# Performance work log

Measured on AMD Instinct MI355X. Metric: run time of the kernel, lower is better.

## Reference

```python
import jax, jax.numpy as jnp
import numpy as np

B, A, N = 4, 256, 64
NCB, NF, NSB, DIMS = 128, 128, 50, 3
CUTOFF = 5.0
LOG2 = 0.6931471805599453


def ssp(x):
    # shifted softplus: softplus(x) - ln(2)
    return jax.nn.softplus(x) - LOG2


def mlp2(x, W1, b1, W2, b2):
    # Dense(act=ssp) -> Dense(linear)
    return ssp(x @ W1 + b1) @ W2 + b2


def setup_inputs():
    key = jax.random.key(0)
    ks = jax.random.split(key, 32)

    def w(k, shape):
        return jax.random.normal(k, shape, jnp.float32) / np.sqrt(shape[0]).astype(np.float32)

    return {
        "xi": jax.random.normal(ks[0], (B, A, NCB), jnp.float32),
        "r_ij": jax.random.uniform(ks[1], (B, A, N), jnp.float32) * CUTOFF,
        "cos_ij": jax.random.normal(ks[2], (B, A, N, DIMS), jnp.float32),
        "f_ij": jax.random.normal(ks[3], (B, A, N, NSB), jnp.float32),
        "neighbor_mask": jnp.ones((B, A, N), jnp.float32),
        "filt_W1": w(ks[4], (NSB, NF)), "filt_b1": jnp.zeros((NF,), jnp.float32),
        "filt_W2": w(ks[5], (NF, NF)), "filt_b2": jnp.zeros((NF,), jnp.float32),
        "in2f_W": w(ks[6], (NCB, NF)),
        "f2out_W": w(ks[7], (NF, NF)), "f2out_b": jnp.zeros((NF,), jnp.float32),
        "atom_W1": w(ks[8], (NF, NF)), "atom_b1": jnp.zeros((NF,), jnp.float32),
        "atom_W2": w(ks[9], (NF, NCB)), "atom_b2": jnp.zeros((NCB,), jnp.float32),
        "pair_W1": w(ks[10], (NF, NF)), "pair_b1": jnp.zeros((NF,), jnp.float32),
        "pair_W2": w(ks[11], (NF, NCB)), "pair_b2": jnp.zeros((NCB,), jnp.float32),
        "env_W1": w(ks[12], (NF, NF)), "env_b1": jnp.zeros((NF,), jnp.float32),
        "env_W2": w(ks[13], (NF, NCB)), "env_b2": jnp.zeros((NCB,), jnp.float32),
        "neighbors": jax.random.randint(ks[14], (B, A, N), 0, A),
    }


def reference(xi, r_ij, cos_ij, f_ij, neighbor_mask,
              filt_W1, filt_b1, filt_W2, filt_b2, in2f_W, f2out_W, f2out_b,
              atom_W1, atom_b1, atom_W2, atom_b2,
              pair_W1, pair_b1, pair_W2, pair_b2,
              env_W1, env_b1, env_W2, env_b2, neighbors):
    bidx = jnp.arange(B)[:, None, None]
    # --- FTLayer: filter net on Gaussian-expanded distances, cosine cutoff ---
    Wf = ssp(f_ij @ filt_W1 + filt_b1) @ filt_W2 + filt_b2            # [B,A,N,NF]
    C = 0.5 * (jnp.cos(r_ij * (jnp.pi / CUTOFF)) + 1.0) * (r_ij < CUTOFF)
    Wf = Wf * C[..., None]
    yj = (xi @ in2f_W)[bidx, neighbors]                               # gather -> [B,A,N,NF]
    v = ssp((yj * Wf) @ f2out_W + f2out_b)                            # [B,A,N,NF]
    # --- atom-wise channel (masked neighbor sum) ---
    vi = jnp.sum(v * neighbor_mask[..., None], axis=2)                # [B,A,NF]
    vi = mlp2(vi, atom_W1, atom_b1, atom_W2, atom_b2)                 # [B,A,NCB]
    # --- pair tensor: outer product with cosine basis ---
    vij = mlp2(v, pair_W1, pair_b1, pair_W2, pair_b2)                 # [B,A,N,NCB]
    Vij = vij[..., None] * cos_ij[..., None, :]                       # [B,A,N,NCB,3]
    # --- environment tensor: masked agg then second-order neighbor gather ---
    vik = mlp2(v, env_W1, env_b1, env_W2, env_b2)                     # [B,A,N,NCB]
    Vik = jnp.sum(vik[..., None] * cos_ij[..., None, :]
                  * neighbor_mask[..., None, None], axis=2)           # [B,A,NCB,3]
    Vjl = Vik[bidx, neighbors]                                        # [B,A,N,NCB,3]
    V = Vij + Vik[:, :, None] + Vjl                                   # [B,A,N,NCB,3]
    return vi, V
```

## Files before the change

kernel.cpp:

```cpp
#include <hip/hip_runtime.h>
#include <hip/hip_bf16.h>
#include <math.h>

#define B 4
#define A 256
#define NN 64
#define NCB 128
#define NF 128
#define NSB 50
#define BA (B*A)
#define PAIRS (BA*NN)

typedef __bf16 bf;
typedef __attribute__((ext_vector_type(8))) __bf16 bfrag8;
typedef __attribute__((ext_vector_type(4))) float ffrag4;

__device__ __attribute__((aligned(16))) bf    g_yib[BA*NF];
__device__ __attribute__((aligned(16))) bf    g_vij[(size_t)PAIRS*NCB];
__device__ __attribute__((aligned(16))) float g_vik[BA*NCB*3];
__device__ __attribute__((aligned(16))) bf g_tf1[NF*64];
__device__ __attribute__((aligned(16))) bf g_tf2[NF*NF];
__device__ __attribute__((aligned(16))) bf g_tfo[NF*NF];
__device__ __attribute__((aligned(16))) bf g_tp1[NF*NF];
__device__ __attribute__((aligned(16))) bf g_tp2[NF*NF];
__device__ __attribute__((aligned(16))) bf g_te1[NF*NF];
__device__ __attribute__((aligned(16))) bf g_te2[NF*NF];

__device__ __forceinline__ float ssp(float x){
    float e = __expf(-fabsf(x));
    return fmaxf(x, 0.f) + __logf(1.f + e) - 0.6931471805599453f;
}

__global__ __launch_bounds__(256)
void k_wt(const float* __restrict__ f1, const float* __restrict__ f2,
          const float* __restrict__ fo, const float* __restrict__ p1,
          const float* __restrict__ p2, const float* __restrict__ e1,
          const float* __restrict__ e2){
    int s = blockIdx.x >> 3, part = blockIdx.x & 7;
    const float* src; bf* dst; int kb, realK;
    if (s == 0){ src = f1; dst = g_tf1; kb = 6; realK = NSB; }
    else {
        kb = 7; realK = 128;
        src = (s==1)?f2:(s==2)?fo:(s==3)?p1:(s==4)?p2:(s==5)?e1:e2;
        dst = (s==1)?g_tf2:(s==2)?g_tfo:(s==3)?g_tp1:(s==4)?g_tp2:(s==5)?g_te1:g_te2;
    }
    int total = NF << kb;
    int chunk = total >> 3;
    int end = (part + 1) * chunk;
    for (int e = part*chunk + threadIdx.x; e < end; e += 256){
        int n = e >> kb, k = e & ((1<<kb)-1);
        dst[e] = (k < realK) ? (bf)src[k*NF + n] : (bf)0.f;
    }
}

__global__ __launch_bounds__(NF)
void k_yi(const float* __restrict__ xi, const float* __restrict__ W){
    int row = blockIdx.x, f = threadIdx.x;
    __shared__ float x[NCB];
    x[f] = xi[row*NCB + f];
    __syncthreads();
    float s = 0.f;
    #pragma unroll 16
    for (int c = 0; c < NCB; c++) s += x[c]*W[c*NF + f];
    g_yib[row*NF + f] = (bf)s;
}

__device__ __forceinline__ void stage_w128(bf* __restrict__ sW, const bf* __restrict__ g,
                                           int half, int tid){
    #pragma unroll
    for (int i = 0; i < 4; i++){
        int r  = i*16 + (tid >> 4);
        int cp = (tid & 15)*8;
        *(bfrag8*)&sW[r*136 + cp] = *(const bfrag8*)&g[(half*64 + r)*128 + cp];
    }
}
__device__ __forceinline__ void stage_w64(bf* __restrict__ sW, const bf* __restrict__ g,
                                          int half, int tid){
    #pragma unroll
    for (int i = 0; i < 2; i++){
        int r  = i*32 + (tid >> 3);
        int cp = (tid & 7)*8;
        *(bfrag8*)&sW[r*72 + cp] = *(const bfrag8*)&g[(half*64 + r)*64 + cp];
    }
}
__device__ __forceinline__ void gemm4(const bf* __restrict__ sW, const bfrag8 afr[4],
                                      ffrag4 acc[4], int q, int c16){
    #pragma unroll
    for (int nt = 0; nt < 4; nt++){
        ffrag4 a = {0.f,0.f,0.f,0.f};
        #pragma unroll
        for (int kt = 0; kt < 4; kt++){
            bfrag8 bv = *(const bfrag8*)&sW[(nt*16 + c16)*136 + kt*32 + q*8];
            a = __builtin_amdgcn_mfma_f32_16x16x32_bf16(afr[kt], bv, a, 0, 0, 0);
        }
        acc[nt] = a;
    }
}
__device__ __forceinline__ void gemm2(const bf* __restrict__ sW, const bfrag8 afr[2],
                                      ffrag4 acc[4], int q, int c16){
    #pragma unroll
    for (int nt = 0; nt < 4; nt++){
        ffrag4 a = {0.f,0.f,0.f,0.f};
        #pragma unroll
        for (int kt = 0; kt < 2; kt++){
            bfrag8 bv = *(const bfrag8*)&sW[(nt*16 + c16)*72 + kt*32 + q*8];
            a = __builtin_amdgcn_mfma_f32_16x16x32_bf16(afr[kt], bv, a, 0, 0, 0);
        }
        acc[nt] = a;
    }
}

__global__ __launch_bounds__(256, 3)
void k_main(const float* __restrict__ r_ij, const float* __restrict__ cos_ij,
            const float* __restrict__ f_ij, const float* __restrict__ mask,
            const int* __restrict__ neighbors,
            const float* __restrict__ fb1, const float* __restrict__ fb2,
            const float* __restrict__ f2b,
            const float* __restrict__ aW1, const float* __restrict__ ab1,
            const float* __restrict__ aW2, const float* __restrict__ ab2,
            const float* __restrict__ pb1, const float* __restrict__ pb2,
            const float* __restrict__ eb1, const float* __restrict__ eb2,
            float* __restrict__ out_vi){
    const int tid  = threadIdx.x;
    const int ba   = blockIdx.x;
    const int b    = ba >> 8;
    const int w    = tid >> 6;
    const int lane = tid & 63;
    const int q    = lane >> 4;
    const int c16  = lane & 15;
    const int arow = w*16 + c16;

    __shared__ __attribute__((aligned(16))) char sWb[64*136*2];
    bf* const sW = (bf*)sWb;
    __shared__ __attribute__((aligned(16))) bf sA [64*136];
    __shared__ __attribute__((aligned(16))) bf sA2[64*136];
    __shared__ float sCosM[64*4];
    __shared__ float sCr[64];
    __shared__ int   sJb[64];

    #pragma unroll
    for (int i = 0; i < 16; i++){
        int e = tid + i*256;
        int row = e >> 6, col = e & 63;
        float v = (col < NSB) ? f_ij[(ba*64 + row)*NSB + col] : 0.f;
        sA2[row*136 + col] = (bf)v;
    }
    if (tid < 64){
        int p = ba*64 + tid;
        sCosM[tid*4+0] = cos_ij[p*3+0];
        sCosM[tid*4+1] = cos_ij[p*3+1];
        sCosM[tid*4+2] = cos_ij[p*3+2];
        sCosM[tid*4+3] = mask[p];
        float r = r_ij[p];
        sCr[tid] = (r < 5.f) ? 0.5f*(__cosf(r*0.62831853071795864769f) + 1.f) : 0.f;
        int j = neighbors[p] & (A-1);
        sJb[tid] = (b*A + j)*NF;
    }
    __syncthreads();

    bfrag8 afr4[4]; bfrag8 afr2[2]; ffrag4 acc[4];

    #pragma unroll
    for (int kt = 0; kt < 2; kt++) afr2[kt] = *(const bfrag8*)&sA2[arow*136 + kt*32 + q*8];
    #pragma unroll
    for (int half = 0; half < 2; half++){
        if (half) __syncthreads();
        stage_w64(sW, g_tf1, half, tid);
        __syncthreads();
        gemm2(sW, afr2, acc, q, c16);
        #pragma unroll
        for (int nt = 0; nt < 4; nt++){
            int col = (half*4 + nt)*16 + c16;
            float bias = fb1[col];
            #pragma unroll
            for (int rg = 0; rg < 4; rg++){
                int row = w*16 + q*4 + rg;
                sA[row*136 + col] = (bf)ssp(acc[nt][rg] + bias);
            }
        }
    }
    __syncthreads();

    #pragma unroll
    for (int kt = 0; kt < 4; kt++) afr4[kt] = *(const bfrag8*)&sA[arow*136 + kt*32 + q*8];
    #pragma unroll
    for (int half = 0; half < 2; half++){
        if (half) __syncthreads();
        stage_w128(sW, g_tf2, half, tid);
        __syncthreads();
        gemm4(sW, afr4, acc, q, c16);
        #pragma unroll
        for (int nt = 0; nt < 4; nt++){
            int col = (half*4 + nt)*16 + c16;
            float bias = fb2[col];
            #pragma unroll
            for (int rg = 0; rg < 4; rg++){
                int row = w*16 + q*4 + rg;
                float wf = (acc[nt][rg] + bias) * sCr[row];
                float u  = (float)g_yib[sJb[row] + col] * wf;
                sA[row*136 + col] = (bf)u;
            }
        }
    }
    __syncthreads();

    float vsAll[8];
    #pragma unroll
    for (int t = 0; t < 8; t++) vsAll[t] = 0.f;
    #pragma unroll
    for (int kt = 0; kt < 4; kt++) afr4[kt] = *(const bfrag8*)&sA[arow*136 + kt*32 + q*8];
    #pragma unroll
    for (int half = 0; half < 2; half++){
        if (half) __syncthreads();
        stage_w128(sW, g_tfo, half, tid);
        __syncthreads();
        gemm4(sW, afr4, acc, q, c16);
        #pragma unroll
        for (int nt = 0; nt < 4; nt++){
            int col = (half*4 + nt)*16 + c16;
            float bias = f2b[col];
            #pragma unroll
            for (int rg = 0; rg < 4; rg++){
                int row = w*16 + q*4 + rg;
                float v = ssp(acc[nt][rg] + bias);
                sA[row*136 + col] = (bf)v;
                vsAll[half*4 + nt] += v * sCosM[row*4+3];
            }
        }
    }
    __syncthreads();

    #pragma unroll
    for (int kt = 0; kt < 4; kt++) afr4[kt] = *(const bfrag8*)&sA[arow*136 + kt*32 + q*8];
    #pragma unroll
    for (int half = 0; half < 2; half++){
        if (half) __syncthreads();
        stage_w128(sW, g_tp1, half, tid);
        __syncthreads();
        gemm4(sW, afr4, acc, q, c16);
        #pragma unroll
        for (int nt = 0; nt < 4; nt++){
            int col = (half*4 + nt)*16 + c16;
            float bias = pb1[col];
            #pragma unroll
            for (int rg = 0; rg < 4; rg++){
                int row = w*16 + q*4 + rg;
                sA2[row*136 + col] = (bf)ssp(acc[nt][rg] + bias);
            }
        }
    }
    __syncthreads();

    #pragma unroll
    for (int kt = 0; kt < 4; kt++) afr4[kt] = *(const bfrag8*)&sA2[arow*136 + kt*32 + q*8];
    #pragma unroll
    for (int half = 0; half < 2; half++){
        if (half) __syncthreads();
        stage_w128(sW, g_tp2, half, tid);
        __syncthreads();
        gemm4(sW, afr4, acc, q, c16);
        #pragma unroll
        for (int nt = 0; nt < 4; nt++){
            int col = (half*4 + nt)*16 + c16;
            float bias = pb2[col];
            #pragma unroll
            for (int rg = 0; rg < 4; rg++){
                int row = w*16 + q*4 + rg;
                sA2[row*136 + col] = (bf)(acc[nt][rg] + bias);
            }
        }
    }
    __syncthreads();

    #pragma unroll
    for (int i = 0; i < 4; i++){
        int row = i*16 + (tid >> 4);
        int cp  = (tid & 15)*8;
        *(bfrag8*)&g_vij[((size_t)ba*64 + row)*128 + cp] = *(const bfrag8*)&sA2[row*136 + cp];
    }
    #pragma unroll
    for (int kt = 0; kt < 4; kt++) afr4[kt] = *(const bfrag8*)&sA[arow*136 + kt*32 + q*8];
    #pragma unroll
    for (int half = 0; half < 2; half++){
        if (half) __syncthreads();
        stage_w128(sW, g_te1, half, tid);
        __syncthreads();
        gemm4(sW, afr4, acc, q, c16);
        #pragma unroll
        for (int nt = 0; nt < 4; nt++){
            int col = (half*4 + nt)*16 + c16;
            float bias = eb1[col];
            #pragma unroll
            for (int rg = 0; rg < 4; rg++){
                int row = w*16 + q*4 + rg;
                sA2[row*136 + col] = (bf)ssp(acc[nt][rg] + bias);
            }
        }
    }
    __syncthreads();

    float vkAll[8][3];
    #pragma unroll
    for (int t = 0; t < 8; t++){ vkAll[t][0]=0.f; vkAll[t][1]=0.f; vkAll[t][2]=0.f; }
    #pragma unroll
    for (int kt = 0; kt < 4; kt++) afr4[kt] = *(const bfrag8*)&sA2[arow*136 + kt*32 + q*8];
    #pragma unroll
    for (int half = 0; half < 2; half++){
        if (half) __syncthreads();
        stage_w128(sW, g_te2, half, tid);
        __syncthreads();
        gemm4(sW, afr4, acc, q, c16);
        #pragma unroll
        for (int nt = 0; nt < 4; nt++){
            float bias = eb2[(half*4 + nt)*16 + c16];
            #pragma unroll
            for (int rg = 0; rg < 4; rg++){
                int row = w*16 + q*4 + rg;
                float vik = (acc[nt][rg] + bias) * sCosM[row*4+3];
                vkAll[half*4 + nt][0] += vik * sCosM[row*4+0];
                vkAll[half*4 + nt][1] += vik * sCosM[row*4+1];
                vkAll[half*4 + nt][2] += vik * sCosM[row*4+2];
            }
        }
    }

    __syncthreads();
    float* const sVs   = (float*)sWb;
    float* const sVk   = (float*)(sWb + 2048);
    float* const sVsum = (float*)(sWb + 8192);
    float* const sHa   = (float*)(sWb + 8704);
    #pragma unroll
    for (int t = 0; t < 8; t++){
        float v = vsAll[t];
        v += __shfl_xor(v, 16);
        v += __shfl_xor(v, 32);
        if (q == 0) sVs[w*128 + t*16 + c16] = v;
    }
    #pragma unroll
    for (int t = 0; t < 8; t++){
        #pragma unroll
        for (int d = 0; d < 3; d++){
            float v = vkAll[t][d];
            v += __shfl_xor(v, 16);
            v += __shfl_xor(v, 32);
            if (q == 0) sVk[w*384 + (t*16 + c16)*3 + d] = v;
        }
    }
    __syncthreads();

    for (int e = tid; e < 384; e += 256)
        g_vik[ba*384 + e] = sVk[e] + sVk[384+e] + sVk[768+e] + sVk[1152+e];
    if (tid < 128)
        sVsum[tid] = sVs[tid] + sVs[128+tid] + sVs[256+tid] + sVs[384+tid];
    __syncthreads();
    if (tid < 128){
        float acc2 = ab1[tid];
        #pragma unroll 16
        for (int k = 0; k < 128; k++) acc2 += sVsum[k]*aW1[k*128 + tid];
        sHa[tid] = ssp(acc2);
    }
    __syncthreads();
    if (tid < 128){
        float acc2 = ab2[tid];
        #pragma unroll 16
        for (int k = 0; k < 128; k++) acc2 += sHa[k]*aW2[k*128 + tid];
        out_vi[ba*128 + tid] = acc2;
    }
}

__global__ __launch_bounds__(256)
void k_V(const float* __restrict__ cos_ij, const int* __restrict__ nbrs,
         float* __restrict__ outV){
    const int ba  = blockIdx.x;
    const int b   = ba >> 8;
    const int tid = threadIdx.x;
    const int g   = tid >> 7;
    const int t   = tid & 127;
    __shared__ float sVa[384];
    __shared__ float sC[64*3];
    __shared__ int   sJ[64];
    for (int e = tid; e < 384; e += 256) sVa[e] = g_vik[ba*384 + e];
    if (tid < 64){
        int p = ba*64 + tid;
        sJ[tid] = (b*A + (nbrs[p] & (A-1)))*384;
        sC[tid*3+0] = cos_ij[p*3+0];
        sC[tid*3+1] = cos_ij[p*3+1];
        sC[tid*3+2] = cos_ij[p*3+2];
    }
    __syncthreads();
    const int t3 = t*3;
    const float a0 = sVa[t3+0], a1 = sVa[t3+1], a2 = sVa[t3+2];
    #pragma unroll 2
    for (int i = 0; i < 32; i++){
        int n = i*2 + g;
        size_t p = (size_t)ba*64 + n;
        float vv = (float)g_vij[p*128 + t];
        const float* vjp = g_vik + sJ[n] + t3;
        float c0 = sC[n*3+0], c1 = sC[n*3+1], c2 = sC[n*3+2];
        float* o = outV + p*384 + t3;
        __builtin_nontemporal_store(fmaf(vv, c0, a0 + vjp[0]), o+0);
        __builtin_nontemporal_store(fmaf(vv, c1, a1 + vjp[1]), o+1);
        __builtin_nontemporal_store(fmaf(vv, c2, a2 + vjp[2]), o+2);
    }
}

extern "C" void kernel_launch(void* const* d_in, const int* in_sizes, int n_in,
                              void* d_out, int out_size, void* d_ws, size_t ws_size,
                              hipStream_t stream){
    const float* xi      = (const float*)d_in[0];
    const float* r_ij    = (const float*)d_in[1];
    const float* cos_ij  = (const float*)d_in[2];
    const float* f_ij    = (const float*)d_in[3];
    const float* nmask   = (const float*)d_in[4];
    const float* fW1     = (const float*)d_in[5];
    const float* fb1     = (const float*)d_in[6];
    const float* fW2     = (const float*)d_in[7];
    const float* fb2     = (const float*)d_in[8];
    const float* in2f_W  = (const float*)d_in[9];
    const float* f2W     = (const float*)d_in[10];
    const float* f2b     = (const float*)d_in[11];
    const float* aW1     = (const float*)d_in[12];
    const float* ab1     = (const float*)d_in[13];
    const float* aW2     = (const float*)d_in[14];
    const float* ab2     = (const float*)d_in[15];
    const float* pW1     = (const float*)d_in[16];
    const float* pb1     = (const float*)d_in[17];
    const float* pW2     = (const float*)d_in[18];
    const float* pb2     = (const float*)d_in[19];
    const float* eW1     = (const float*)d_in[20];
    const float* eb1     = (const float*)d_in[21];
    const float* eW2     = (const float*)d_in[22];
    const float* eb2     = (const float*)d_in[23];
    const int*  nbrs     = (const int*)d_in[24];

    float* out_vi = (float*)d_out;
    float* outV   = (float*)d_out + BA*NCB;

    k_wt<<<56, 256, 0, stream>>>(fW1, fW2, f2W, pW1, pW2, eW1, eW2);
    k_yi<<<BA, NF, 0, stream>>>(xi, in2f_W);

    k_main<<<BA, 256, 0, stream>>>(r_ij, cos_ij, f_ij, nmask, nbrs,
                                   fb1, fb2, f2b,
                                   aW1, ab1, aW2, ab2,
                                   pb1, pb2, eb1, eb2,
                                   out_vi);

    k_V<<<BA, 256, 0, stream>>>(cos_ij, nbrs, outV);
}
```

Measured before the change: 258.3 us.

## Shrink LDS to two buffers, keep activations in registers, vectorize V writer

k_main drops from three 17KB LDS buffers to two by keeping the v activation fragments in registers (afrV) and reusing them for both the pair and env MLPs. Operand fragments are read before the barrier, so one scratch buffer can be overwritten in place. The launch bound rises from 3 to 4 blocks per CU. k_V now stages the vij tile in LDS and writes the output with 16-byte nontemporal vector stores instead of scalar stores. The trade-off is more register pressure from the extra fragment array, and some per-element div/mod index math in k_V.

```diff
diff --git a/kernel.cpp b/kernel.cpp
--- a/kernel.cpp
+++ b/kernel.cpp
@@ -110,7 +110,28 @@
     }
 }
 
-__global__ __launch_bounds__(256, 3)
+#define RDA4(DST) { _Pragma("unroll") for (int kt = 0; kt < 4; kt++) \
+    DST[kt] = *(const bfrag8*)&sX[arow*136 + kt*32 + q*8]; }
+
+#define EPI_SSP(BIASP, H) \
+    { _Pragma("unroll") for (int nt = 0; nt < 4; nt++){ \
+        int col = ((H)*4 + nt)*16 + c16; \
+        float bias = BIASP[col]; \
+        _Pragma("unroll") for (int rg = 0; rg < 4; rg++){ \
+            int row = w*16 + q*4 + rg; \
+            sX[row*136 + col] = (bf)ssp(acc[nt][rg] + bias); \
+        } } }
+
+#define EPI_LIN(BIASP, H) \
+    { _Pragma("unroll") for (int nt = 0; nt < 4; nt++){ \
+        int col = ((H)*4 + nt)*16 + c16; \
+        float bias = BIASP[col]; \
+        _Pragma("unroll") for (int rg = 0; rg < 4; rg++){ \
+            int row = w*16 + q*4 + rg; \
+            sX[row*136 + col] = (bf)(acc[nt][rg] + bias); \
+        } } }
+
+__global__ __launch_bounds__(256, 4)
 void k_main(const float* __restrict__ r_ij, const float* __restrict__ cos_ij,
             const float* __restrict__ f_ij, const float* __restrict__ mask,
             const int* __restrict__ neighbors,
@@ -130,65 +151,52 @@
     const int c16  = lane & 15;
     const int arow = w*16 + c16;
 
-    __shared__ __attribute__((aligned(16))) char sWb[64*136*2];
-    bf* const sW = (bf*)sWb;
-    __shared__ __attribute__((aligned(16))) bf sA [64*136];
-    __shared__ __attribute__((aligned(16))) bf sA2[64*136];
+    __shared__ __attribute__((aligned(16))) bf sW[64*136];
+    __shared__ __attribute__((aligned(16))) bf sX[64*136];
     __shared__ float sCosM[64*4];
     __shared__ float sCr[64];
     __shared__ int   sJb[64];
 
     #pragma unroll
     for (int i = 0; i < 16; i++){
-        int e = tid + i*256;
-        int row = e >> 6, col = e & 63;
-        float v = (col < NSB) ? f_ij[(ba*64 + row)*NSB + col] : 0.f;
-        sA2[row*136 + col] = (bf)v;
-    }
-    if (tid < 64){
-        int p = ba*64 + tid;
-        sCosM[tid*4+0] = cos_ij[p*3+0];
-        sCosM[tid*4+1] = cos_ij[p*3+1];
-        sCosM[tid*4+2] = cos_ij[p*3+2];
-        sCosM[tid*4+3] = mask[p];
+        int row = w*16 + i;
+        float v = (lane < NSB) ? f_ij[(ba*64 + row)*NSB + lane] : 0.f;
+        sX[row*136 + lane] = (bf)v;
+    }
+    if (lane < 16){
+        int row = w*16 + lane;
+        int p = ba*64 + row;
+        sCosM[row*4+0] = cos_ij[p*3+0];
+        sCosM[row*4+1] = cos_ij[p*3+1];
+        sCosM[row*4+2] = cos_ij[p*3+2];
+        sCosM[row*4+3] = mask[p];
         float r = r_ij[p];
-        sCr[tid] = (r < 5.f) ? 0.5f*(__cosf(r*0.62831853071795864769f) + 1.f) : 0.f;
+        sCr[row] = (r < 5.f) ? 0.5f*(__cosf(r*0.62831853071795864769f) + 1.f) : 0.f;
         int j = neighbors[p] & (A-1);
-        sJb[tid] = (b*A + j)*NF;
-    }
-    __syncthreads();
-
-    bfrag8 afr4[4]; bfrag8 afr2[2]; ffrag4 acc[4];
-
-    #pragma unroll
-    for (int kt = 0; kt < 2; kt++) afr2[kt] = *(const bfrag8*)&sA2[arow*136 + kt*32 + q*8];
+        sJb[row] = (b*A + j)*NF;
+    }
+
+    bfrag8 afr[4], afrV[4], afr2[2]; ffrag4 acc[4];
+
+    #pragma unroll
+    for (int kt = 0; kt < 2; kt++) afr2[kt] = *(const bfrag8*)&sX[arow*136 + kt*32 + q*8];
     #pragma unroll
     for (int half = 0; half < 2; half++){
         if (half) __syncthreads();
         stage_w64(sW, g_tf1, half, tid);
         __syncthreads();
         gemm2(sW, afr2, acc, q, c16);
-        #pragma unroll
-        for (int nt = 0; nt < 4; nt++){
-            int col = (half*4 + nt)*16 + c16;
-            float bias = fb1[col];
-            #pragma unroll
-            for (int rg = 0; rg < 4; rg++){
-                int row = w*16 + q*4 + rg;
-                sA[row*136 + col] = (bf)ssp(acc[nt][rg] + bias);
-            }
-        }
-    }
-    __syncthreads();
-
-    #pragma unroll
-    for (int kt = 0; kt < 4; kt++) afr4[kt] = *(const bfrag8*)&sA[arow*136 + kt*32 + q*8];
+        EPI_SSP(fb1, half);
+    }
+    RDA4(afr);
+    __syncthreads();
+
     #pragma unroll
     for (int half = 0; half < 2; half++){
         if (half) __syncthreads();
         stage_w128(sW, g_tf2, half, tid);
         __syncthreads();
-        gemm4(sW, afr4, acc, q, c16);
+        gemm4(sW, afr, acc, q, c16);
         #pragma unroll
         for (int nt = 0; nt < 4; nt++){
             int col = (half*4 + nt)*16 + c16;
@@ -197,24 +205,22 @@
             for (int rg = 0; rg < 4; rg++){
                 int row = w*16 + q*4 + rg;
                 float wf = (acc[nt][rg] + bias) * sCr[row];
-                float u  = (float)g_yib[sJb[row] + col] * wf;
-                sA[row*136 + col] = (bf)u;
+                sX[row*136 + col] = (bf)((float)g_yib[sJb[row] + col] * wf);
             }
         }
     }
+    RDA4(afr);
     __syncthreads();
 
     float vsAll[8];
     #pragma unroll
     for (int t = 0; t < 8; t++) vsAll[t] = 0.f;
     #pragma unroll
-    for (int kt = 0; kt < 4; kt++) afr4[kt] = *(const bfrag8*)&sA[arow*136 + kt*32 + q*8];
-    #pragma unroll
     for (int half = 0; half < 2; half++){
         if (half) __syncthreads();
         stage_w128(sW, g_tfo, half, tid);
         __syncthreads();
-        gemm4(sW, afr4, acc, q, c16);
+        gemm4(sW, afr, acc, q, c16);
         #pragma unroll
         for (int nt = 0; nt < 4; nt++){
             int col = (half*4 + nt)*16 + c16;
@@ -223,93 +229,61 @@
             for (int rg = 0; rg < 4; rg++){
                 int row = w*16 + q*4 + rg;
                 float v = ssp(acc[nt][rg] + bias);
-                sA[row*136 + col] = (bf)v;
+                sX[row*136 + col] = (bf)v;
                 vsAll[half*4 + nt] += v * sCosM[row*4+3];
             }
         }
     }
-    __syncthreads();
-
-    #pragma unroll
-    for (int kt = 0; kt < 4; kt++) afr4[kt] = *(const bfrag8*)&sA[arow*136 + kt*32 + q*8];
+    RDA4(afrV);
+    __syncthreads();
+
     #pragma unroll
     for (int half = 0; half < 2; half++){
         if (half) __syncthreads();
         stage_w128(sW, g_tp1, half, tid);
         __syncthreads();
-        gemm4(sW, afr4, acc, q, c16);
-        #pragma unroll
-        for (int nt = 0; nt < 4; nt++){
-            int col = (half*4 + nt)*16 + c16;
-            float bias = pb1[col];
-            #pragma unroll
-            for (int rg = 0; rg < 4; rg++){
-                int row = w*16 + q*4 + rg;
-                sA2[row*136 + col] = (bf)ssp(acc[nt][rg] + bias);
-            }
-        }
-    }
-    __syncthreads();
-
-    #pragma unroll
-    for (int kt = 0; kt < 4; kt++) afr4[kt] = *(const bfrag8*)&sA2[arow*136 + kt*32 + q*8];
+        gemm4(sW, afrV, acc, q, c16);
+        EPI_SSP(pb1, half);
+    }
+    RDA4(afr);
+    __syncthreads();
+
     #pragma unroll
     for (int half = 0; half < 2; half++){
         if (half) __syncthreads();
         stage_w128(sW, g_tp2, half, tid);
         __syncthreads();
-        gemm4(sW, afr4, acc, q, c16);
-        #pragma unroll
-        for (int nt = 0; nt < 4; nt++){
-            int col = (half*4 + nt)*16 + c16;
-            float bias = pb2[col];
-            #pragma unroll
-            for (int rg = 0; rg < 4; rg++){
-                int row = w*16 + q*4 + rg;
-                sA2[row*136 + col] = (bf)(acc[nt][rg] + bias);
-            }
-        }
-    }
-    __syncthreads();
-
+        gemm4(sW, afr, acc, q, c16);
+        EPI_LIN(pb2, half);
+    }
     #pragma unroll
     for (int i = 0; i < 4; i++){
-        int row = i*16 + (tid >> 4);
-        int cp  = (tid & 15)*8;
-        *(bfrag8*)&g_vij[((size_t)ba*64 + row)*128 + cp] = *(const bfrag8*)&sA2[row*136 + cp];
-    }
-    #pragma unroll
-    for (int kt = 0; kt < 4; kt++) afr4[kt] = *(const bfrag8*)&sA[arow*136 + kt*32 + q*8];
+        int row = w*16 + i*4 + (lane >> 4);
+        int cp  = c16*8;
+        *(bfrag8*)&g_vij[((size_t)ba*64 + row)*128 + cp] = *(const bfrag8*)&sX[row*136 + cp];
+    }
+    __syncthreads();
+
     #pragma unroll
     for (int half = 0; half < 2; half++){
         if (half) __syncthreads();
         stage_w128(sW, g_te1, half, tid);
         __syncthreads();
-        gemm4(sW, afr4, acc, q, c16);
-        #pragma unroll
-        for (int nt = 0; nt < 4; nt++){
-            int col = (half*4 + nt)*16 + c16;
-            float bias = eb1[col];
-            #pragma unroll
-            for (int rg = 0; rg < 4; rg++){
-                int row = w*16 + q*4 + rg;
-                sA2[row*136 + col] = (bf)ssp(acc[nt][rg] + bias);
-            }
-        }
-    }
+        gemm4(sW, afrV, acc, q, c16);
+        EPI_SSP(eb1, half);
+    }
+    RDA4(afr);
     __syncthreads();
 
     float vkAll[8][3];
     #pragma unroll
     for (int t = 0; t < 8; t++){ vkAll[t][0]=0.f; vkAll[t][1]=0.f; vkAll[t][2]=0.f; }
     #pragma unroll
-    for (int kt = 0; kt < 4; kt++) afr4[kt] = *(const bfrag8*)&sA2[arow*136 + kt*32 + q*8];
-    #pragma unroll
     for (int half = 0; half < 2; half++){
         if (half) __syncthreads();
         stage_w128(sW, g_te2, half, tid);
         __syncthreads();
-        gemm4(sW, afr4, acc, q, c16);
+        gemm4(sW, afr, acc, q, c16);
         #pragma unroll
         for (int nt = 0; nt < 4; nt++){
             float bias = eb2[(half*4 + nt)*16 + c16];
@@ -325,10 +299,10 @@
     }
 
     __syncthreads();
-    float* const sVs   = (float*)sWb;
-    float* const sVk   = (float*)(sWb + 2048);
-    float* const sVsum = (float*)(sWb + 8192);
-    float* const sHa   = (float*)(sWb + 8704);
+    float* const sVs   = (float*)sX;
+    float* const sVk   = (float*)((char*)sX + 2048);
+    float* const sVsum = (float*)((char*)sX + 8192);
+    float* const sHa   = (float*)((char*)sX + 8704);
     #pragma unroll
     for (int t = 0; t < 8; t++){
         float v = vsAll[t];
@@ -374,33 +348,42 @@
     const int ba  = blockIdx.x;
     const int b   = ba >> 8;
     const int tid = threadIdx.x;
-    const int g   = tid >> 7;
-    const int t   = tid & 127;
+    __shared__ __attribute__((aligned(16))) bf sVij[64*128];
     __shared__ float sVa[384];
-    __shared__ float sC[64*3];
+    __shared__ float sC[64*4];
     __shared__ int   sJ[64];
+    #pragma unroll
+    for (int i = 0; i < 4; i++){
+        int e8 = tid + i*256;
+        *(bfrag8*)&sVij[e8*8] = *(const bfrag8*)&g_vij[(size_t)ba*8192 + e8*8];
+    }
     for (int e = tid; e < 384; e += 256) sVa[e] = g_vik[ba*384 + e];
     if (tid < 64){
         int p = ba*64 + tid;
         sJ[tid] = (b*A + (nbrs[p] & (A-1)))*384;
-        sC[tid*3+0] = cos_ij[p*3+0];
-        sC[tid*3+1] = cos_ij[p*3+1];
-        sC[tid*3+2] = cos_ij[p*3+2];
-    }
-    __syncthreads();
-    const int t3 = t*3;
-    const float a0 = sVa[t3+0], a1 = sVa[t3+1], a2 = sVa[t3+2];
-    #pragma unroll 2
-    for (int i = 0; i < 32; i++){
-        int n = i*2 + g;
-        size_t p = (size_t)ba*64 + n;
-        float vv = (float)g_vij[p*128 + t];
-        const float* vjp = g_vik + sJ[n] + t3;
-        float c0 = sC[n*3+0], c1 = sC[n*3+1], c2 = sC[n*3+2];
-        float* o = outV + p*384 + t3;
-        __builtin_nontemporal_store(fmaf(vv, c0, a0 + vjp[0]), o+0);
-        __builtin_nontemporal_store(fmaf(vv, c1, a1 + vjp[1]), o+1);
-        __builtin_nontemporal_store(fmaf(vv, c2, a2 + vjp[2]), o+2);
+        sC[tid*4+0] = cos_ij[p*3+0];
+        sC[tid*4+1] = cos_ij[p*3+1];
+        sC[tid*4+2] = cos_ij[p*3+2];
+    }
+    __syncthreads();
+    float* const oBase = outV + (size_t)ba*24576;
+    #pragma unroll 4
+    for (int it = 0; it < 24; it++){
+        int idx = (it*256 + tid)*4;
+        int pl  = idx / 384;
+        int e0  = idx - pl*384;
+        ffrag4 va = *(const ffrag4*)&sVa[e0];
+        ffrag4 vj = *(const ffrag4*)(g_vik + sJ[pl] + e0);
+        ffrag4 o;
+        #pragma unroll
+        for (int j2 = 0; j2 < 4; j2++){
+            int e = e0 + j2;
+            int c = e / 3;
+            int d = e - c*3;
+            float vv = (float)sVij[pl*128 + c];
+            o[j2] = fmaf(vv, sC[pl*4+d], va[j2] + vj[j2]);
+        }
+        __builtin_nontemporal_store(o, (ffrag4*)(oBase + idx));
     }
 }
 
```

Result: faster. 235.8 us (-8.7%).
